# Kernel optimization log

Hardware: AMD Instinct MI355X
Metric: run time of the kernel (lower is better)

The kernel has to match this reference:

```python
import jax, jax.numpy as jnp
import numpy as np

N, E, D = 10000, 160000, 256
EPS = 1e-5


def layer_norm(x, gamma, beta):
    mu = jnp.mean(x, axis=-1, keepdims=True)
    var = jnp.var(x, axis=-1, keepdims=True)
    return (x - mu) * jax.lax.rsqrt(var + EPS) * gamma + beta


def mlp(x, w1, b1, w2, b2):
    return jax.nn.relu(x @ w1 + b1) @ w2 + b2


def setup_inputs() -> dict:
    key = jax.random.key(0)
    ks = jax.random.split(key, 16)
    s = lambda fan_in: 1.0 / np.sqrt(fan_in)
    inp = {
        'x': jax.random.normal(ks[0], (N, D), jnp.float32),
        'edge_index': jax.random.randint(ks[1], (2, E), 0, N, jnp.int64),
        'edge_attr': jax.random.normal(ks[2], (E, D), jnp.float32),
        # edge MLP: in 3D=768 -> hidden 2D=512 -> out D=256, then LN
        'e_w1': jax.random.uniform(ks[3], (3 * D, 2 * D), jnp.float32, -s(3 * D), s(3 * D)),
        'e_b1': jnp.zeros((2 * D,), jnp.float32),
        'e_w2': jax.random.uniform(ks[4], (2 * D, D), jnp.float32, -s(2 * D), s(2 * D)),
        'e_b2': jnp.zeros((D,), jnp.float32),
        'e_g': jnp.ones((D,), jnp.float32),
        'e_beta': jnp.zeros((D,), jnp.float32),
        # node MLP: in 2D=512 -> hidden 2D=512 -> out D=256, then LN
        'n_w1': jax.random.uniform(ks[5], (2 * D, 2 * D), jnp.float32, -s(2 * D), s(2 * D)),
        'n_b1': jnp.zeros((2 * D,), jnp.float32),
        'n_w2': jax.random.uniform(ks[6], (2 * D, D), jnp.float32, -s(2 * D), s(2 * D)),
        'n_b2': jnp.zeros((D,), jnp.float32),
        'n_g': jnp.ones((D,), jnp.float32),
        'n_beta': jnp.zeros((D,), jnp.float32),
    }
    return inp


def reference(x, edge_index, edge_attr, e_w1, e_b1, e_w2, e_b2, e_g, e_beta,
              n_w1, n_b1, n_w2, n_b2, n_g, n_beta):
    i, j = edge_index[0], edge_index[1]
    # Edge processor: gather, concat, MLP + LN, residual
    h = jnp.concatenate([x[i], x[j], edge_attr], axis=-1)  # [E, 3D]
    new_edge = edge_attr + layer_norm(mlp(h, e_w1, e_b1, e_w2, e_b2), e_g, e_beta)
    # Node processor: scatter-add over j, concat, MLP + LN, residual
    agg = jax.ops.segment_sum(new_edge, j, num_segments=x.shape[0])  # [N, D]
    hn = jnp.concatenate([x, agg], axis=-1)  # [N, 2D]
    new_x = x + layer_norm(mlp(hn, n_w1, n_b1, n_w2, n_b2), n_g, n_beta)
    return new_x, new_edge
```

## Files before the change

kernel.cpp:

```cpp
#include <hip/hip_runtime.h>

#define NNODE 10000
#define NEDGE 160000
#define DD 256

using f32x4  = __attribute__((ext_vector_type(4))) float;
using bf16x8 = __attribute__((ext_vector_type(8))) short;
using u32x4  = __attribute__((ext_vector_type(4))) unsigned;

__device__ inline short f2bf(float f) {
  unsigned u = __float_as_uint(f);
  unsigned r = (u + 0x7fffu + ((u >> 16) & 1u)) >> 16;
  return (short)(unsigned short)r;
}

__device__ inline float bf2f(short s) {
  return __uint_as_float(((unsigned)(unsigned short)s) << 16);
}

__device__ inline unsigned pkbf(float a, float b) {
  unsigned r;
  asm("v_cvt_pk_bf16_f32 %0, %1, %2" : "=v"(r) : "v"(a), "v"(b));
  return r;
}

__global__ void cast_x_kernel(const float* __restrict__ x, short* __restrict__ xb, int total) {
  int i = blockIdx.x * 256 + threadIdx.x;
  if (i < total) xb[i] = f2bf(x[i]);
}

__global__ void pack_w_kernel(const float* __restrict__ w, short* __restrict__ p, int K, int N) {
  int idx = blockIdx.x * 256 + threadIdx.x;
  if (idx >= K * N) return;
  int k = idx / N, n = idx - k * N;
  p[(size_t)(k >> 3) * N * 8 + (size_t)n * 8 + (k & 7)] = f2bf(w[idx]);
}

__global__ void pack_ew1_kernel(const float* __restrict__ w, short* __restrict__ w1abp,
                                short* __restrict__ w1cp) {
  int idx = blockIdx.x * 256 + threadIdx.x;
  if (idx >= 768 * 512) return;
  int k = idx >> 9, n = idx & 511;
  short v = f2bf(w[idx]);
  if (k < 256) {
    w1abp[(size_t)(k >> 3) * 1024 * 8 + (size_t)n * 8 + (k & 7)] = v;
  } else if (k < 512) {
    int kk = k - 256;
    w1abp[(size_t)(kk >> 3) * 1024 * 8 + (size_t)(512 + n) * 8 + (kk & 7)] = v;
  } else {
    int kk = k - 512;
    w1cp[(size_t)(kk >> 3) * 512 * 8 + (size_t)n * 8 + (kk & 7)] = v;
  }
}

__global__ void hist_kernel(const int* __restrict__ ei, int* __restrict__ deg) {
  int e = blockIdx.x * 256 + threadIdx.x;
  if (e < NEDGE) {
    int j = ei[NEDGE + e]; j = min(max(j, 0), NNODE - 1);
    atomicAdd(&deg[j], 1);
  }
}

__global__ void scan_kernel(const int* __restrict__ deg, int* __restrict__ row_start) {
  __shared__ int part[256];
  int t = threadIdx.x;
  const int CH = 40;
  int base = t * CH;
  int s = 0;
  for (int i = 0; i < CH; i++) {
    int idx = base + i;
    s += (idx < NNODE) ? deg[idx] : 0;
  }
  part[t] = s;
  __syncthreads();
  for (int off = 1; off < 256; off <<= 1) {
    int v = (t >= off) ? part[t - off] : 0;
    __syncthreads();
    part[t] += v;
    __syncthreads();
  }
  int run = (t == 0) ? 0 : part[t - 1];
  for (int i = 0; i < CH; i++) {
    int idx = base + i;
    if (idx < NNODE) { row_start[idx] = run; run += deg[idx]; }
  }
  if (t == 255) row_start[NNODE] = part[255];
}

__global__ void scatter_kernel(const int* __restrict__ ei, const int* __restrict__ row_start,
                               int* __restrict__ cursor, int* __restrict__ csr) {
  int e = blockIdx.x * 256 + threadIdx.x;
  if (e < NEDGE) {
    int j = ei[NEDGE + e]; j = min(max(j, 0), NNODE - 1);
    int p = atomicAdd(&cursor[j], 1);
    csr[row_start[j] + p] = e;
  }
}

__global__ __launch_bounds__(256) void agg_kernel(const float* __restrict__ out_e,
                                                  const int* __restrict__ row_start,
                                                  const int* __restrict__ csr,
                                                  short* __restrict__ aggb) {
  int node = blockIdx.x * 4 + (threadIdx.x >> 6);
  int lane = threadIdx.x & 63;
  if (node >= NNODE) return;
  int rs = row_start[node], re = row_start[node + 1];
  float4 acc = {0.f, 0.f, 0.f, 0.f};
  for (int k = rs; k < re; k++) {
    int eid = csr[k];
    float4 v = *(const float4*)(out_e + (size_t)eid * DD + lane * 4);
    acc.x += v.x; acc.y += v.y; acc.z += v.z; acc.w += v.w;
  }
  short4 o;
  o.x = f2bf(acc.x); o.y = f2bf(acc.y); o.z = f2bf(acc.z); o.w = f2bf(acc.w);
  *(short4*)(aggb + (size_t)node * DD + lane * 4) = o;
}

__global__ __launch_bounds__(256, 2)
void precomp_pab(const short* __restrict__ xb, const short* __restrict__ w1abp,
                 short* __restrict__ pab) {
  __shared__ __align__(16) short abuf[2048 * 8];

  const int tid  = threadIdx.x;
  const int lane = tid & 63;
  const int wid  = tid >> 6;
  const int lhi  = lane >> 4;
  const int llo  = lane & 15;
  const int swz  = llo & 7;
  const int m0   = blockIdx.x * 64;
  const int h    = blockIdx.y;

  #pragma unroll
  for (int q = 0; q < 8; q++) {
    int S = wid * 512 + q * 64 + lane;
    int row = S >> 5;
    int segp = S & 31;
    int seg = segp ^ (row & 7);
    int rowg = min(m0 + row, NNODE - 1);
    __builtin_amdgcn_global_load_lds(
        (const int*)((const char*)xb + (size_t)rowg * 512 + seg * 16),
        (int*)(abuf + (size_t)(wid * 512 + q * 64) * 8), 16, 0, 0);
  }
  __syncthreads();

  f32x4 acc1[4][8] = {};
  const bf16x8* bp1 = (const bf16x8*)w1abp;
  #pragma unroll
  for (int kk = 0; kk < 256; kk += 32) {
    const int ks = kk >> 3;
    bf16x8 a[4];
    #pragma unroll
    for (int mf = 0; mf < 4; mf++)
      a[mf] = *(const bf16x8*)(abuf + ((mf * 16 + llo) * 32 + ((ks + lhi) ^ swz)) * 8);
    const bf16x8* bb = bp1 + (size_t)(ks + lhi) * 1024 + h * 512 + wid * 128 + llo;
    #pragma unroll
    for (int nf = 0; nf < 8; nf++) {
      bf16x8 b = bb[nf * 16];
      #pragma unroll
      for (int mf = 0; mf < 4; mf++)
        acc1[mf][nf] = __builtin_amdgcn_mfma_f32_16x16x32_bf16(a[mf], b, acc1[mf][nf], 0, 0, 0);
    }
  }

  #pragma unroll
  for (int mf = 0; mf < 4; mf++) {
    #pragma unroll
    for (int r = 0; r < 4; r++) {
      int row = m0 + mf * 16 + lhi * 4 + r;
      if (row < NNODE) {
        u32x4 wv = { pkbf(acc1[mf][0][r], acc1[mf][1][r]),
                     pkbf(acc1[mf][2][r], acc1[mf][3][r]),
                     pkbf(acc1[mf][4][r], acc1[mf][5][r]),
                     pkbf(acc1[mf][6][r], acc1[mf][7][r]) };
        *(u32x4*)(pab + (size_t)row * 1024 + h * 512 + llo * 32 + wid * 8) = wv;
      }
    }
  }
}

__global__ __launch_bounds__(256, 2)
void fused_edge(const int* __restrict__ ei,
                const int* __restrict__ csr,
                const float* __restrict__ ea,
                const short* __restrict__ pab,
                const short* __restrict__ w1cp,
                const float* __restrict__ b1,
                const short* __restrict__ w2p,
                const float* __restrict__ b2,
                const float* __restrict__ gam,
                const float* __restrict__ bet,
                float* __restrict__ out)
{
  __shared__ __align__(16) short hid[64 * 512];
  __shared__ int eidx[64], idxi[64], idxj[64];
  __shared__ float pS[256], pQ[256];

  short* abuf = hid;

  const int tid  = threadIdx.x;
  const int lane = tid & 63;
  const int wid  = tid >> 6;
  const int lhi  = lane >> 4;
  const int llo  = lane & 15;
  const int swz  = llo & 7;
  const int m0   = blockIdx.x * 64;

  if (tid < 64) {
    int e = csr[m0 + tid];
    eidx[tid] = e;
    int a = ei[e];
    int b = ei[NEDGE + e];
    idxi[tid] = min(max(a, 0), NNODE - 1);
    idxj[tid] = min(max(b, 0), NNODE - 1);
  }
  __syncthreads();

  #pragma unroll
  for (int q = 0; q < 8; q++) {
    int S = q * 256 + tid;
    int row = S >> 5;
    int segp = S & 31;
    int seg = segp ^ (row & 7);
    const float* src = ea + (size_t)eidx[row] * 256 + seg * 8;
    float4 u0 = *(const float4*)src;
    float4 u1 = *(const float4*)(src + 4);
    u32x4 qv = { pkbf(u0.x, u0.y), pkbf(u0.z, u0.w), pkbf(u1.x, u1.y), pkbf(u1.z, u1.w) };
    *(u32x4*)(abuf + (size_t)S * 8) = qv;
  }
  __syncthreads();

  f32x4 acc1[4][8] = {};
  const bf16x8* bp1 = (const bf16x8*)w1cp;
  #pragma unroll
  for (int kk = 0; kk < 256; kk += 32) {
    const int ks = kk >> 3;
    bf16x8 a[4];
    #pragma unroll
    for (int mf = 0; mf < 4; mf++)
      a[mf] = *(const bf16x8*)(abuf + ((mf * 16 + llo) * 32 + ((ks + lhi) ^ swz)) * 8);
    const bf16x8* bb = bp1 + (size_t)(ks + lhi) * 512 + wid * 128 + llo;
    #pragma unroll
    for (int nf = 0; nf < 8; nf++) {
      bf16x8 b = bb[nf * 16];
      #pragma unroll
      for (int mf = 0; mf < 4; mf++)
        acc1[mf][nf] = __builtin_amdgcn_mfma_f32_16x16x32_bf16(a[mf], b, acc1[mf][nf], 0, 0, 0);
    }
  }

  #pragma unroll
  for (int mf = 0; mf < 4; mf++) {
    #pragma unroll
    for (int r = 0; r < 4; r++) {
      int row = mf * 16 + lhi * 4 + r;
      int gi = idxi[row], gj = idxj[row];
      bf16x8 pa = *(const bf16x8*)(pab + (size_t)gi * 1024 + llo * 32 + wid * 8);
      bf16x8 pb = *(const bf16x8*)(pab + (size_t)gj * 1024 + 512 + llo * 32 + wid * 8);
      #pragma unroll
      for (int nf = 0; nf < 8; nf++)
        acc1[mf][nf][r] += bf2f(pa[nf]) + bf2f(pb[nf]);
    }
  }
  __syncthreads();

  #pragma unroll
  for (int nf = 0; nf < 8; nf++) {
    int col = wid * 128 + nf * 16 + llo;
    float bb = b1[col];
    int cs = col >> 3, cl = col & 7;
    #pragma unroll
    for (int mf = 0; mf < 4; mf++) {
      #pragma unroll
      for (int r = 0; r < 4; r++) {
        int row = mf * 16 + lhi * 4 + r;
        float v = acc1[mf][nf][r] + bb;
        v = v > 0.f ? v : 0.f;
        hid[row * 512 + ((cs ^ (row & 7)) * 8) + cl] = f2bf(v);
      }
    }
  }
  __syncthreads();

  f32x4 acc2[4][4] = {};
  const bf16x8* bp2 = (const bf16x8*)w2p;
  const int bcol2 = wid * 64 + llo;
  #pragma unroll
  for (int kk = 0; kk < 512; kk += 32) {
    const int ks = kk >> 3;
    bf16x8 a[4];
    #pragma unroll
    for (int mf = 0; mf < 4; mf++) {
      int row = mf * 16 + llo;
      a[mf] = *(const bf16x8*)(hid + row * 512 + (((ks + lhi) ^ swz) * 8));
    }
    const bf16x8* bb = bp2 + (size_t)(ks + lhi) * 256 + bcol2;
    #pragma unroll
    for (int nf = 0; nf < 4; nf++) {
      bf16x8 b = bb[nf * 16];
      #pragma unroll
      for (int mf = 0; mf < 4; mf++)
        acc2[mf][nf] = __builtin_amdgcn_mfma_f32_16x16x32_bf16(a[mf], b, acc2[mf][nf], 0, 0, 0);
    }
  }

  float bb2[4], gg[4], be[4];
  #pragma unroll
  for (int nf = 0; nf < 4; nf++) {
    int col = bcol2 + nf * 16;
    bb2[nf] = b2[col]; gg[nf] = gam[col]; be[nf] = bet[col];
  }
  #pragma unroll
  for (int mf = 0; mf < 4; mf++)
    #pragma unroll
    for (int nf = 0; nf < 4; nf++)
      #pragma unroll
      for (int r = 0; r < 4; r++)
        acc2[mf][nf][r] += bb2[nf];

  float S[4][4], Q[4][4];
  #pragma unroll
  for (int mf = 0; mf < 4; mf++) {
    #pragma unroll
    for (int r = 0; r < 4; r++) {
      float s = 0.f, q = 0.f;
      #pragma unroll
      for (int nf = 0; nf < 4; nf++) {
        float v = acc2[mf][nf][r];
        s += v; q += v * v;
      }
      S[mf][r] = s; Q[mf][r] = q;
    }
  }
  #pragma unroll
  for (int m = 1; m <= 8; m <<= 1) {
    #pragma unroll
    for (int mf = 0; mf < 4; mf++)
      #pragma unroll
      for (int r = 0; r < 4; r++) {
        S[mf][r] += __shfl_xor(S[mf][r], m);
        Q[mf][r] += __shfl_xor(Q[mf][r], m);
      }
  }
  if (llo == 0) {
    #pragma unroll
    for (int mf = 0; mf < 4; mf++)
      #pragma unroll
      for (int r = 0; r < 4; r++) {
        int row = mf * 16 + lhi * 4 + r;
        pS[wid * 64 + row] = S[mf][r];
        pQ[wid * 64 + row] = Q[mf][r];
      }
  }
  __syncthreads();

  float mu[4][4], rsv[4][4];
  #pragma unroll
  for (int mf = 0; mf < 4; mf++) {
    #pragma unroll
    for (int r = 0; r < 4; r++) {
      int row = mf * 16 + lhi * 4 + r;
      float s = pS[row] + pS[64 + row] + pS[128 + row] + pS[192 + row];
      float q = pQ[row] + pQ[64 + row] + pQ[128 + row] + pQ[192 + row];
      float m_ = s * (1.f / 256.f);
      mu[mf][r]  = m_;
      rsv[mf][r] = rsqrtf(q * (1.f / 256.f) - m_ * m_ + 1e-5f);
    }
  }

  #pragma unroll
  for (int mf = 0; mf < 4; mf++) {
    #pragma unroll
    for (int r = 0; r < 4; r++) {
      int erow = eidx[mf * 16 + lhi * 4 + r];
      const float* rp = ea  + (size_t)erow * DD + bcol2;
      float*       op = out + (size_t)erow * DD + bcol2;
      #pragma unroll
      for (int nf = 0; nf < 4; nf++) {
        float v = (acc2[mf][nf][r] - mu[mf][r]) * rsv[mf][r] * gg[nf] + be[nf] + rp[nf * 16];
        op[nf * 16] = v;
      }
    }
  }
}

__global__ __launch_bounds__(256, 2)
void fused_node(const float* __restrict__ x,
                const short* __restrict__ xb,
                const short* __restrict__ aggb,
                const short* __restrict__ w1p,
                const float* __restrict__ b1,
                const short* __restrict__ w2p,
                const float* __restrict__ b2,
                const float* __restrict__ gam,
                const float* __restrict__ bet,
                float* __restrict__ out)
{
  constexpr int HP = 520;
  __shared__ __align__(16) short hid[64 * HP];
  __shared__ float pS[4][64], pQ[4][64];

  const int tid  = threadIdx.x;
  const int lane = tid & 63;
  const int wid  = tid >> 6;
  const int m0   = blockIdx.x * 64;
  const int lhi  = lane >> 4;
  const int llo  = lane & 15;

  const short* pI[4]; const short* pJ[4];
  #pragma unroll
  for (int mf = 0; mf < 4; mf++) {
    int rr = min(m0 + mf * 16 + llo, NNODE - 1);
    pI[mf] = xb + (size_t)rr * DD;
    pJ[mf] = aggb + (size_t)rr * DD;
  }

  f32x4 acc1[4][8] = {};
  const bf16x8* bp1 = (const bf16x8*)w1p;
  const int bcol1 = wid * 128 + llo;

  #pragma unroll
  for (int s = 0; s < 8; s++) {
    #pragma unroll
    for (int kk = 0; kk < 64; kk += 32) {
      const int ko = s * 64 + kk + lhi * 8;
      bf16x8 a[4];
      #pragma unroll
      for (int mf = 0; mf < 4; mf++) {
        if (s < 4) a[mf] = *(const bf16x8*)(pI[mf] + ko);
        else       a[mf] = *(const bf16x8*)(pJ[mf] + (ko - 256));
      }
      const bf16x8* bb = bp1 + (size_t)(s * 8 + (kk >> 3) + lhi) * 512 + bcol1;
      #pragma unroll
      for (int nf = 0; nf < 8; nf++) {
        bf16x8 b = bb[nf * 16];
        #pragma unroll
        for (int mf = 0; mf < 4; mf++)
          acc1[mf][nf] = __builtin_amdgcn_mfma_f32_16x16x32_bf16(a[mf], b, acc1[mf][nf], 0, 0, 0);
      }
    }
  }

  #pragma unroll
  for (int nf = 0; nf < 8; nf++) {
    int col = wid * 128 + nf * 16 + llo;
    float bb = b1[col];
    #pragma unroll
    for (int mf = 0; mf < 4; mf++) {
      #pragma unroll
      for (int r = 0; r < 4; r++) {
        float v = acc1[mf][nf][r] + bb;
        v = v > 0.f ? v : 0.f;
        hid[(mf * 16 + lhi * 4 + r) * HP + col] = f2bf(v);
      }
    }
  }
  __syncthreads();

  f32x4 acc2[4][4] = {};
  const bf16x8* bp2 = (const bf16x8*)w2p;
  const int bcol2 = wid * 64 + llo;
  #pragma unroll
  for (int kk = 0; kk < 512; kk += 32) {
    bf16x8 a[4];
    #pragma unroll
    for (int mf = 0; mf < 4; mf++)
      a[mf] = *(const bf16x8*)(hid + (mf * 16 + llo) * HP + kk + lhi * 8);
    const bf16x8* bb = bp2 + (size_t)((kk >> 3) + lhi) * 256 + bcol2;
    #pragma unroll
    for (int nf = 0; nf < 4; nf++) {
      bf16x8 b = bb[nf * 16];
      #pragma unroll
      for (int mf = 0; mf < 4; mf++)
        acc2[mf][nf] = __builtin_amdgcn_mfma_f32_16x16x32_bf16(a[mf], b, acc2[mf][nf], 0, 0, 0);
    }
  }

  float bb2[4], gg[4], be[4];
  #pragma unroll
  for (int nf = 0; nf < 4; nf++) {
    int col = bcol2 + nf * 16;
    bb2[nf] = b2[col]; gg[nf] = gam[col]; be[nf] = bet[col];
  }
  #pragma unroll
  for (int mf = 0; mf < 4; mf++)
    #pragma unroll
    for (int nf = 0; nf < 4; nf++)
      #pragma unroll
      for (int r = 0; r < 4; r++)
        acc2[mf][nf][r] += bb2[nf];

  float S[4][4], Q[4][4];
  #pragma unroll
  for (int mf = 0; mf < 4; mf++) {
    #pragma unroll
    for (int r = 0; r < 4; r++) {
      float s = 0.f, q = 0.f;
      #pragma unroll
      for (int nf = 0; nf < 4; nf++) {
        float v = acc2[mf][nf][r];
        s += v; q += v * v;
      }
      S[mf][r] = s; Q[mf][r] = q;
    }
  }
  #pragma unroll
  for (int m = 1; m <= 8; m <<= 1) {
    #pragma unroll
    for (int mf = 0; mf < 4; mf++)
      #pragma unroll
      for (int r = 0; r < 4; r++) {
        S[mf][r] += __shfl_xor(S[mf][r], m);
        Q[mf][r] += __shfl_xor(Q[mf][r], m);
      }
  }
  if (llo == 0) {
    #pragma unroll
    for (int mf = 0; mf < 4; mf++)
      #pragma unroll
      for (int r = 0; r < 4; r++) {
        int row = mf * 16 + lhi * 4 + r;
        pS[wid][row] = S[mf][r];
        pQ[wid][row] = Q[mf][r];
      }
  }
  __syncthreads();

  float mu[4][4], rsv[4][4];
  #pragma unroll
  for (int mf = 0; mf < 4; mf++) {
    #pragma unroll
    for (int r = 0; r < 4; r++) {
      int row = mf * 16 + lhi * 4 + r;
      float s = pS[0][row] + pS[1][row] + pS[2][row] + pS[3][row];
      float q = pQ[0][row] + pQ[1][row] + pQ[2][row] + pQ[3][row];
      float m_ = s * (1.f / 256.f);
      mu[mf][r]  = m_;
      rsv[mf][r] = rsqrtf(q * (1.f / 256.f) - m_ * m_ + 1e-5f);
    }
  }

  #pragma unroll
  for (int mf = 0; mf < 4; mf++) {
    #pragma unroll
    for (int r = 0; r < 4; r++) {
      int grow = m0 + mf * 16 + lhi * 4 + r;
      if (grow >= NNODE) continue;
      const float* rp = x   + (size_t)grow * DD + bcol2;
      float*       op = out + (size_t)grow * DD + bcol2;
      #pragma unroll
      for (int nf = 0; nf < 4; nf++) {
        float v = (acc2[mf][nf][r] - mu[mf][r]) * rsv[mf][r] * gg[nf] + be[nf] + rp[nf * 16];
        op[nf * 16] = v;
      }
    }
  }
}

extern "C" void kernel_launch(void* const* d_in, const int* in_sizes, int n_in,
                              void* d_out, int out_size, void* d_ws, size_t ws_size,
                              hipStream_t stream) {
  const float* x      = (const float*)d_in[0];
  const int*   ei     = (const int*)  d_in[1];
  const float* ea     = (const float*)d_in[2];
  const float* e_w1   = (const float*)d_in[3];
  const float* e_b1   = (const float*)d_in[4];
  const float* e_w2   = (const float*)d_in[5];
  const float* e_b2   = (const float*)d_in[6];
  const float* e_g    = (const float*)d_in[7];
  const float* e_beta = (const float*)d_in[8];
  const float* n_w1   = (const float*)d_in[9];
  const float* n_b1   = (const float*)d_in[10];
  const float* n_w2   = (const float*)d_in[11];
  const float* n_b2   = (const float*)d_in[12];
  const float* n_g    = (const float*)d_in[13];
  const float* n_beta = (const float*)d_in[14];

  float* out_x = (float*)d_out;
  float* out_e = (float*)d_out + (size_t)NNODE * DD;

  char* w = (char*)d_ws;
  short* xb    = (short*)(w);
  short* aggb  = (short*)(w + 5120000);
  short* pab   = (short*)(w + 10240000);
  short* w1abp = (short*)(w + 30720000);
  short* w1cp  = (short*)(w + 31244288);
  short* ew2p  = (short*)(w + 31506432);
  short* nw1p  = (short*)(w + 31768576);
  short* nw2p  = (short*)(w + 32292864);
  int*   deg   = (int*)  (w + 32555008);
  int*   cur   = (int*)  (w + 32595968);
  int*   rs    = (int*)  (w + 32636928);
  int*   csr   = (int*)  (w + 32677904);

  hipMemsetAsync(deg, 0, 81920, stream);

  cast_x_kernel<<<(NNODE * DD + 255) / 256, 256, 0, stream>>>(x, xb, NNODE * DD);
  pack_ew1_kernel<<<(768 * 512 + 255) / 256, 256, 0, stream>>>(e_w1, w1abp, w1cp);
  pack_w_kernel<<<(512 * 512 + 255) / 256, 256, 0, stream>>>(n_w1, nw1p, 512, 512);
  pack_w_kernel<<<(512 * 256 + 255) / 256, 256, 0, stream>>>(e_w2, ew2p, 512, 256);
  pack_w_kernel<<<(512 * 256 + 255) / 256, 256, 0, stream>>>(n_w2, nw2p, 512, 256);

  hist_kernel<<<(NEDGE + 255) / 256, 256, 0, stream>>>(ei, deg);
  scan_kernel<<<1, 256, 0, stream>>>(deg, rs);
  scatter_kernel<<<(NEDGE + 255) / 256, 256, 0, stream>>>(ei, rs, cur, csr);

  precomp_pab<<<dim3((NNODE + 63) / 64, 2), 256, 0, stream>>>(xb, w1abp, pab);

  fused_edge<<<NEDGE / 64, 256, 0, stream>>>(ei, csr, ea, pab, w1cp, e_b1,
                                             ew2p, e_b2, e_g, e_beta, out_e);
  agg_kernel<<<(NNODE + 3) / 4, 256, 0, stream>>>(out_e, rs, csr, aggb);
  fused_node<<<(NNODE + 63) / 64, 256, 0, stream>>>(x, xb, aggb, nw1p, n_b1,
                                                    nw2p, n_b2, n_g, n_beta, out_x);
}
```

Baseline: 529.0 us.

## Fuse scatter-add aggregation into edge kernel via segmented atomics

Measured after the change: 474.2 us. -10.4%, faster.

```diff
diff --git a/kernel.cpp b/kernel.cpp
--- a/kernel.cpp
+++ b/kernel.cpp
@@ -97,25 +97,6 @@
   }
 }
 
-__global__ __launch_bounds__(256) void agg_kernel(const float* __restrict__ out_e,
-                                                  const int* __restrict__ row_start,
-                                                  const int* __restrict__ csr,
-                                                  short* __restrict__ aggb) {
-  int node = blockIdx.x * 4 + (threadIdx.x >> 6);
-  int lane = threadIdx.x & 63;
-  if (node >= NNODE) return;
-  int rs = row_start[node], re = row_start[node + 1];
-  float4 acc = {0.f, 0.f, 0.f, 0.f};
-  for (int k = rs; k < re; k++) {
-    int eid = csr[k];
-    float4 v = *(const float4*)(out_e + (size_t)eid * DD + lane * 4);
-    acc.x += v.x; acc.y += v.y; acc.z += v.z; acc.w += v.w;
-  }
-  short4 o;
-  o.x = f2bf(acc.x); o.y = f2bf(acc.y); o.z = f2bf(acc.z); o.w = f2bf(acc.w);
-  *(short4*)(aggb + (size_t)node * DD + lane * 4) = o;
-}
-
 __global__ __launch_bounds__(256, 2)
 void precomp_pab(const short* __restrict__ xb, const short* __restrict__ w1abp,
                  short* __restrict__ pab) {
@@ -189,13 +170,16 @@
                 const float* __restrict__ b2,
                 const float* __restrict__ gam,
                 const float* __restrict__ bet,
-                float* __restrict__ out)
+                float* __restrict__ out,
+                float* __restrict__ aggf)
 {
-  __shared__ __align__(16) short hid[64 * 512];
+  __shared__ __align__(16) char smem[66560];
   __shared__ int eidx[64], idxi[64], idxj[64];
   __shared__ float pS[256], pQ[256];
 
-  short* abuf = hid;
+  short* abuf = (short*)smem;
+  short* hid  = (short*)smem;
+  float* outt = (float*)smem;
 
   const int tid  = threadIdx.x;
   const int lane = tid & 63;
@@ -222,8 +206,8 @@
     int segp = S & 31;
     int seg = segp ^ (row & 7);
     const float* src = ea + (size_t)eidx[row] * 256 + seg * 8;
-    float4 u0 = *(const float4*)src;
-    float4 u1 = *(const float4*)(src + 4);
+    f32x4 u0 = *(const f32x4*)src;
+    f32x4 u1 = *(const f32x4*)(src + 4);
     u32x4 qv = { pkbf(u0.x, u0.y), pkbf(u0.z, u0.w), pkbf(u1.x, u1.y), pkbf(u1.z, u1.w) };
     *(u32x4*)(abuf + (size_t)S * 8) = qv;
   }
@@ -371,22 +355,49 @@
   for (int mf = 0; mf < 4; mf++) {
     #pragma unroll
     for (int r = 0; r < 4; r++) {
-      int erow = eidx[mf * 16 + lhi * 4 + r];
-      const float* rp = ea  + (size_t)erow * DD + bcol2;
-      float*       op = out + (size_t)erow * DD + bcol2;
+      int row = mf * 16 + lhi * 4 + r;
       #pragma unroll
       for (int nf = 0; nf < 4; nf++) {
-        float v = (acc2[mf][nf][r] - mu[mf][r]) * rsv[mf][r] * gg[nf] + be[nf] + rp[nf * 16];
-        op[nf * 16] = v;
-      }
-    }
+        float v = (acc2[mf][nf][r] - mu[mf][r]) * rsv[mf][r] * gg[nf] + be[nf];
+        outt[row * 260 + bcol2 + nf * 16] = v;
+      }
+    }
+  }
+  __syncthreads();
+
+  #pragma unroll
+  for (int it = 0; it < 16; it++) {
+    int row = it * 4 + wid;
+    int e = eidx[row];
+    f32x4 resid = *((const f32x4*)(ea + (size_t)e * 256) + lane);
+    f32x4 o4 = *((const f32x4*)(outt + row * 260) + lane);
+    o4 += resid;
+    __builtin_nontemporal_store(o4, (f32x4*)(out + (size_t)e * 256) + lane);
+    *((f32x4*)(outt + row * 260) + lane) = o4;
+  }
+  __syncthreads();
+
+  {
+    int c = tid;
+    float acc = 0.f;
+    int cj = idxj[0];
+    #pragma unroll 8
+    for (int r = 0; r < 64; r++) {
+      int jr = idxj[r];
+      if (jr != cj) {
+        atomicAdd(&aggf[(size_t)cj * 256 + c], acc);
+        acc = 0.f; cj = jr;
+      }
+      acc += outt[r * 260 + c];
+    }
+    atomicAdd(&aggf[(size_t)cj * 256 + c], acc);
   }
 }
 
 __global__ __launch_bounds__(256, 2)
 void fused_node(const float* __restrict__ x,
                 const short* __restrict__ xb,
-                const short* __restrict__ aggb,
+                const float* __restrict__ aggf,
                 const short* __restrict__ w1p,
                 const float* __restrict__ b1,
                 const short* __restrict__ w2p,
@@ -406,12 +417,12 @@
   const int lhi  = lane >> 4;
   const int llo  = lane & 15;
 
-  const short* pI[4]; const short* pJ[4];
+  const short* pI[4]; const float* pJ[4];
   #pragma unroll
   for (int mf = 0; mf < 4; mf++) {
     int rr = min(m0 + mf * 16 + llo, NNODE - 1);
     pI[mf] = xb + (size_t)rr * DD;
-    pJ[mf] = aggb + (size_t)rr * DD;
+    pJ[mf] = aggf + (size_t)rr * DD;
   }
 
   f32x4 acc1[4][8] = {};
@@ -426,8 +437,16 @@
       bf16x8 a[4];
       #pragma unroll
       for (int mf = 0; mf < 4; mf++) {
-        if (s < 4) a[mf] = *(const bf16x8*)(pI[mf] + ko);
-        else       a[mf] = *(const bf16x8*)(pJ[mf] + (ko - 256));
+        if (s < 4) {
+          a[mf] = *(const bf16x8*)(pI[mf] + ko);
+        } else {
+          const float* fp = pJ[mf] + (ko - 256);
+          f32x4 u0 = *(const f32x4*)fp;
+          f32x4 u1 = *(const f32x4*)(fp + 4);
+          u32x4 q = { pkbf(u0.x, u0.y), pkbf(u0.z, u0.w),
+                      pkbf(u1.x, u1.y), pkbf(u1.z, u1.w) };
+          a[mf] = __builtin_bit_cast(bf16x8, q);
+        }
       }
       const bf16x8* bb = bp1 + (size_t)(s * 8 + (kk >> 3) + lhi) * 512 + bcol1;
       #pragma unroll
@@ -580,19 +599,20 @@
 
   char* w = (char*)d_ws;
   short* xb    = (short*)(w);
-  short* aggb  = (short*)(w + 5120000);
-  short* pab   = (short*)(w + 10240000);
-  short* w1abp = (short*)(w + 30720000);
-  short* w1cp  = (short*)(w + 31244288);
-  short* ew2p  = (short*)(w + 31506432);
-  short* nw1p  = (short*)(w + 31768576);
-  short* nw2p  = (short*)(w + 32292864);
-  int*   deg   = (int*)  (w + 32555008);
-  int*   cur   = (int*)  (w + 32595968);
-  int*   rs    = (int*)  (w + 32636928);
-  int*   csr   = (int*)  (w + 32677904);
+  short* pab   = (short*)(w + 5120000);
+  short* w1abp = (short*)(w + 25600000);
+  short* w1cp  = (short*)(w + 26124288);
+  short* ew2p  = (short*)(w + 26386432);
+  short* nw1p  = (short*)(w + 26648576);
+  short* nw2p  = (short*)(w + 27172864);
+  float* aggf  = (float*)(w + 27435008);
+  int*   deg   = (int*)  (w + 37675008);
+  int*   cur   = (int*)  (w + 37715968);
+  int*   rs    = (int*)  (w + 37756928);
+  int*   csr   = (int*)  (w + 37797904);
 
   hipMemsetAsync(deg, 0, 81920, stream);
+  hipMemsetAsync(aggf, 0, (size_t)NNODE * DD * sizeof(float), stream);
 
   cast_x_kernel<<<(NNODE * DD + 255) / 256, 256, 0, stream>>>(x, xb, NNODE * DD);
   pack_ew1_kernel<<<(768 * 512 + 255) / 256, 256, 0, stream>>>(e_w1, w1abp, w1cp);
@@ -607,8 +627,7 @@
   precomp_pab<<<dim3((NNODE + 63) / 64, 2), 256, 0, stream>>>(xb, w1abp, pab);
 
   fused_edge<<<NEDGE / 64, 256, 0, stream>>>(ei, csr, ea, pab, w1cp, e_b1,
-                                             ew2p, e_b2, e_g, e_beta, out_e);
-  agg_kernel<<<(NNODE + 3) / 4, 256, 0, stream>>>(out_e, rs, csr, aggb);
-  fused_node<<<(NNODE + 63) / 64, 256, 0, stream>>>(x, xb, aggb, nw1p, n_b1,
+                                             ew2p, e_b2, e_g, e_beta, out_e, aggf);
+  fused_node<<<(NNODE + 63) / 64, 256, 0, stream>>>(x, xb, aggf, nw1p, n_b1,
                                                     nw2p, n_b2, n_g, n_beta, out_x);
 }
```
